# Kernel tuning notes

Measured on AMD Instinct MI355X. Metric: run time of the kernel, lower is better.

Reference implementation:

```python
import jax, jax.numpy as jnp
import numpy as np

B, N, D, H = 4, 2048, 768, 12
DK = D // H  # 64

def setup_inputs() -> dict:
    key = jax.random.key(0)
    ks = jax.random.split(key, 7)
    f = lambda k, shape: jax.random.normal(k, shape, dtype=jnp.float32)
    return {
        "Q": f(ks[0], (B, N, D)),
        "K": f(ks[1], (B, N, D)),
        "V": f(ks[2], (B, N, D)),
        "w_q": f(ks[3], (D, D)) * 0.02,
        "w_k": f(ks[4], (D, D)) * 0.02,
        "w_v": f(ks[5], (D, D)) * 0.02,
        "w_o": f(ks[6], (D, D)) * 0.02,
    }

def reference(Q, K, V, w_q, w_k, w_v, w_o):
    # Linear with bias=False: y = x @ W.T, W is [out, in]
    def proj(x, w):
        # [B, N, D] -> [B, H, N, DK]
        y = jnp.einsum('bnd,ed->bne', x, w)
        return y.reshape(B, N, H, DK).transpose(0, 2, 1, 3)
    q = proj(Q, w_q)
    k = proj(K, w_k)
    v = proj(V, w_v)
    scale = 1.0 / jnp.sqrt(jnp.float32(DK))
    scores = jnp.einsum('bhqd,bhkd->bhqk', q, k) * scale  # [B,H,N,N]
    weights = jax.nn.softmax(scores, axis=-1)
    out = jnp.einsum('bhqk,bhkd->bhqd', weights, v)  # [B,H,N,DK]
    out = out.transpose(0, 2, 1, 3).reshape(B, N, D)
    return jnp.einsum('bnd,ed->bne', out, w_o)
```

## Files before the change

kernel.cpp:

```cpp
#include <hip/hip_runtime.h>

typedef unsigned short ushortT;
typedef __attribute__((ext_vector_type(8))) short bf16x8;
typedef __attribute__((ext_vector_type(4))) float f32x4;
typedef __attribute__((ext_vector_type(16))) float f32x16;
typedef __attribute__((ext_vector_type(2))) int i32x2;

#define QSCALE 0.18033688011112042f

__device__ __forceinline__ unsigned short f2bf(float f) {
  unsigned int u = __float_as_uint(f);
  u += 0x7FFFu + ((u >> 16) & 1u);
  return (unsigned short)(u >> 16);
}
__device__ __forceinline__ unsigned short f2bf_fast(float f) {
  unsigned int u = __float_as_uint(f) + 0x8000u;
  return (unsigned short)(u >> 16);
}

__device__ __forceinline__ void gl16(const void* g, void* l) {
  __builtin_amdgcn_global_load_lds(
      (const __attribute__((address_space(1))) void*)g,
      (__attribute__((address_space(3))) void*)l, 16, 0, 0);
}

__device__ __forceinline__ unsigned cvtpk(float lo, float hi) {
  unsigned r;
  asm("v_cvt_pk_bf16_f32 %0, %1, %2" : "=v"(r) : "v"(lo), "v"(hi));
  return r;
}

__global__ __launch_bounds__(256) void cvt_w(
    const float* __restrict__ w0, const float* __restrict__ w1,
    const float* __restrict__ w2, const float* __restrict__ w3,
    ushortT* bw0, ushortT* bw1, ushortT* bw2, ushortT* bw3) {
  int t = blockIdx.y;
  const float* src; ushortT* dst;
  switch (t) {
    case 0: src = w0; dst = bw0; break;
    case 1: src = w1; dst = bw1; break;
    case 2: src = w2; dst = bw2; break;
    default: src = w3; dst = bw3; break;
  }
  int i = (blockIdx.x * 256 + threadIdx.x) * 4;
  float4 f = *(const float4*)(src + i);
  ushort4 o = make_ushort4(f2bf(f.x), f2bf(f.y), f2bf(f.z), f2bf(f.w));
  *(ushort4*)(dst + i) = o;
}

__global__ __launch_bounds__(256) void gemm_qkv(
    const float* __restrict__ fxq, const float* __restrict__ fxk,
    const float* __restrict__ fxv,
    const ushortT* __restrict__ bwq, const ushortT* __restrict__ bwk,
    const ushortT* __restrict__ bwv,
    ushortT* qp, ushortT* kp, ushortT* vtp) {
  constexpr int K = 768;
  __shared__ __attribute__((aligned(16))) ushortT As[128 * 32];
  __shared__ __attribute__((aligned(16))) ushortT Bs[128 * 32];
  const int tid = threadIdx.x;
  const int w = tid >> 6, l = tid & 63;
  const int z = blockIdx.z;
  const int d = blockIdx.x;
  const int bx = (d & 7) * 48 + (d >> 3);
  const float*   Fx = (z == 0) ? fxq : (z == 1 ? fxk : fxv);
  const ushortT* Wb = (z == 0) ? bwq : (z == 1 ? bwk : bwv);
  int m0, n0;
  if (z < 2) { m0 = (bx / 6) * 128; n0 = (bx % 6) * 128; }
  else       { m0 = (bx % 6) * 128; n0 = (bx / 6) * 128; }
  const float*   Fb = Fx + (size_t)(z < 2 ? m0 : n0) * K;
  const ushortT* Gb = Wb + (size_t)(z < 2 ? n0 : m0) * K;
  ushortT* Fl = (z < 2) ? As : Bs;
  ushortT* Gl = (z < 2) ? Bs : As;

  f32x4 acc[4][4] = {};
  const int wr = w >> 1, wc = w & 1;
  const int lg = l >> 4, li = l & 15;
  const int srow = tid >> 2, scol = (tid & 3) * 8;

  for (int k0 = 0; k0 < K; k0 += 32) {
    const float* p0 = Fb + (size_t)srow * K + k0 + scol;
    const float* p1 = Fb + (size_t)(64 + srow) * K + k0 + scol;
    float4 a0 = *(const float4*)p0;
    float4 a1 = *(const float4*)(p0 + 4);
    float4 b0 = *(const float4*)p1;
    float4 b1 = *(const float4*)(p1 + 4);
    gl16(Gb + (size_t)srow * K + (k0 + scol),        (char*)Gl + w * 1024);
    gl16(Gb + (size_t)(64 + srow) * K + (k0 + scol), (char*)Gl + 4096 + w * 1024);
    union { unsigned u[4]; bf16x8 v; } pa, pb;
    pa.u[0] = cvtpk(a0.x, a0.y); pa.u[1] = cvtpk(a0.z, a0.w);
    pa.u[2] = cvtpk(a1.x, a1.y); pa.u[3] = cvtpk(a1.z, a1.w);
    pb.u[0] = cvtpk(b0.x, b0.y); pb.u[1] = cvtpk(b0.z, b0.w);
    pb.u[2] = cvtpk(b1.x, b1.y); pb.u[3] = cvtpk(b1.z, b1.w);
    *(bf16x8*)&Fl[srow * 32 + scol]        = pa.v;
    *(bf16x8*)&Fl[(64 + srow) * 32 + scol] = pb.v;
    __syncthreads();
    bf16x8 af[4], bfr[4];
#pragma unroll
    for (int mi = 0; mi < 4; ++mi)
      af[mi] = *(const bf16x8*)&As[(wr * 64 + mi * 16 + li) * 32 + lg * 8];
#pragma unroll
    for (int ni = 0; ni < 4; ++ni)
      bfr[ni] = *(const bf16x8*)&Bs[(wc * 64 + ni * 16 + li) * 32 + lg * 8];
#pragma unroll
    for (int mi = 0; mi < 4; ++mi)
#pragma unroll
      for (int ni = 0; ni < 4; ++ni)
        acc[mi][ni] = __builtin_amdgcn_mfma_f32_16x16x32_bf16(af[mi], bfr[ni], acc[mi][ni], 0, 0, 0);
    __syncthreads();
  }

  const float sc = (z == 0) ? QSCALE : 1.0f;
  ushortT* dst0 = (z == 0) ? qp : kp;
#pragma unroll
  for (int mi = 0; mi < 4; ++mi) {
#pragma unroll
    for (int ni = 0; ni < 4; ++ni) {
#pragma unroll
      for (int r = 0; r < 4; ++r) {
        int m = m0 + wr * 64 + mi * 16 + lg * 4 + r;
        int n = n0 + wc * 64 + ni * 16 + li;
        float val = acc[mi][ni][r];
        if (z < 2) {
          int b = m >> 11, nn = m & 2047, hh = n >> 6, dk = n & 63;
          dst0[(((size_t)(b * 12 + hh)) * 2048 + nn) * 64 + dk] = f2bf_fast(val * sc);
        } else {
          vtp[(size_t)m * 8192 + n] = f2bf_fast(val);
        }
      }
    }
  }
}

__global__ __launch_bounds__(256) void gemm_out(
    const ushortT* __restrict__ A0, const ushortT* __restrict__ B0, float* O0) {
  constexpr int K = 768;
  __shared__ __attribute__((aligned(16))) ushortT As[128 * 32];
  __shared__ __attribute__((aligned(16))) ushortT Bs[128 * 32];
  const int tid = threadIdx.x;
  const int w = tid >> 6, l = tid & 63;
  const int d = blockIdx.x;
  const int flat = (d & 7) * 48 + (d >> 3);
  const int m0 = (flat / 6) * 128, n0 = (flat % 6) * 128;
  const ushortT* Ab = A0 + (size_t)m0 * K;
  const ushortT* Bb = B0 + (size_t)n0 * K;

  f32x4 acc[4][4] = {};
  const int wr = w >> 1, wc = w & 1;
  const int lg = l >> 4, li = l & 15;
  const int srow = tid >> 2, scol = (tid & 3) * 8;

  for (int k0 = 0; k0 < K; k0 += 32) {
    gl16(Ab + (size_t)srow * K + (k0 + scol),        &As[w * 512]);
    gl16(Ab + (size_t)(64 + srow) * K + (k0 + scol), &As[2048 + w * 512]);
    gl16(Bb + (size_t)srow * K + (k0 + scol),        &Bs[w * 512]);
    gl16(Bb + (size_t)(64 + srow) * K + (k0 + scol), &Bs[2048 + w * 512]);
    __syncthreads();
    bf16x8 af[4], bfr[4];
#pragma unroll
    for (int mi = 0; mi < 4; ++mi)
      af[mi] = *(const bf16x8*)&As[(wr * 64 + mi * 16 + li) * 32 + lg * 8];
#pragma unroll
    for (int ni = 0; ni < 4; ++ni)
      bfr[ni] = *(const bf16x8*)&Bs[(wc * 64 + ni * 16 + li) * 32 + lg * 8];
#pragma unroll
    for (int mi = 0; mi < 4; ++mi)
#pragma unroll
      for (int ni = 0; ni < 4; ++ni)
        acc[mi][ni] = __builtin_amdgcn_mfma_f32_16x16x32_bf16(af[mi], bfr[ni], acc[mi][ni], 0, 0, 0);
    __syncthreads();
  }

#pragma unroll
  for (int mi = 0; mi < 4; ++mi)
#pragma unroll
    for (int ni = 0; ni < 4; ++ni)
#pragma unroll
      for (int r = 0; r < 4; ++r) {
        int m = m0 + wr * 64 + mi * 16 + lg * 4 + r;
        int n = n0 + wc * 64 + ni * 16 + li;
        O0[(size_t)m * 768 + n] = acc[mi][ni][r];
      }
}

__global__ __launch_bounds__(256, 3) void attn(
    const ushortT* __restrict__ qp, const ushortT* __restrict__ kp,
    const ushortT* __restrict__ vtp, ushortT* __restrict__ ao) {
  __shared__ __attribute__((aligned(16))) ushortT Ks[128 * 64];
  __shared__ __attribute__((aligned(16))) ushortT Vs[2 * 64 * 64];
  __shared__ __attribute__((aligned(16))) ushortT Ot[4][32 * 72];
  const int tid = threadIdx.x;
  const int w = tid >> 6, l = tid & 63;
  const int lq = l & 31, h = l >> 5;

  const int flat = blockIdx.y * 16 + blockIdx.x;
  const int head = (flat & 7) * 6 + (flat >> 7);
  const int qt = (flat >> 3) & 15;
  const int bb = head / 12, hh = head % 12;
  const size_t hb = (size_t)head * 2048 * 64;
  const int q0 = qt * 128 + w * 32;

  const ushortT* kbase = kp + hb;
  const ushortT* vbase = vtp + (size_t)(hh * 64) * 8192 + (size_t)bb * 2048;

  const int srow8 = l >> 3;
  const int scol = ((l & 7) ^ srow8) << 3;

#define STAGE(kt)                                                              \
  {                                                                            \
    _Pragma("unroll") for (int j = 0; j < 4; ++j) {                            \
      int rk = (w << 5) + (j << 3) + srow8;                                    \
      gl16(kbase + (size_t)((kt) * 128 + rk) * 64 + scol,                      \
           (char*)Ks + ((w << 5) + (j << 3)) * 128);                           \
      int rv = ((w & 1) << 5) + (j << 3) + srow8;                              \
      gl16(vbase + (size_t)rv * 8192 + (kt) * 128 + (w >> 1) * 64 + scol,      \
           (char*)Vs + (w >> 1) * 8192 + (((w & 1) << 5) + (j << 3)) * 128);   \
    }                                                                          \
  }

  bf16x8 bq[4];
#pragma unroll
  for (int c = 0; c < 4; ++c)
    bq[c] = *(const bf16x8*)&qp[hb + (size_t)(q0 + lq) * 64 + c * 16 + h * 8];

  bf16x8 ones;
#pragma unroll
  for (int e = 0; e < 8; ++e) ones[e] = (short)0x3F80;

  f32x16 oa0 = {}, oa1 = {};
  f32x16 asum = {};
  const int lq7 = lq & 7;

  for (int kt = 0; kt < 16; ++kt) {
    STAGE(kt);
    __syncthreads();

#pragma unroll
    for (int khalf = 0; khalf < 2; ++khalf) {
      const char* kbuf = (const char*)Ks + khalf * 8192;
      const char* vbuf = (const char*)Vs + khalf * 8192;

      f32x16 s0 = {}, s1 = {};
      __builtin_amdgcn_s_setprio(1);
#pragma unroll
      for (int c = 0; c < 4; ++c) {
        bf16x8 a0 = *(const bf16x8*)(kbuf + lq * 128 + (((2 * c + h) ^ lq7) << 4));
        s0 = __builtin_amdgcn_mfma_f32_32x32x16_bf16(a0, bq[c], s0, 0, 0, 0);
      }
#pragma unroll
      for (int c = 0; c < 4; ++c) {
        bf16x8 a1 = *(const bf16x8*)(kbuf + (32 + lq) * 128 + (((2 * c + h) ^ lq7) << 4));
        s1 = __builtin_amdgcn_mfma_f32_32x32x16_bf16(a1, bq[c], s1, 0, 0, 0);
      }
      __builtin_amdgcn_s_setprio(0);

#pragma unroll
      for (int r = 0; r < 16; ++r) s0[r] = exp2f(s0[r]);
#pragma unroll
      for (int r = 0; r < 16; ++r) s1[r] = exp2f(s1[r]);

      unsigned c8[16];
#pragma unroll
      for (int n = 0; n < 8; ++n) c8[n]     = cvtpk(s0[2 * n], s0[2 * n + 1]);
#pragma unroll
      for (int n = 0; n < 8; ++n) c8[8 + n] = cvtpk(s1[2 * n], s1[2 * n + 1]);

      __builtin_amdgcn_s_setprio(1);
#pragma unroll
      for (int kcg = 0; kcg < 4; ++kcg) {
        const unsigned* cc = &c8[(kcg >> 1) * 8 + (kcg & 1) * 4];
        i32x2 rA = __builtin_amdgcn_permlane32_swap((int)cc[0], (int)cc[2], false, false);
        i32x2 rB = __builtin_amdgcn_permlane32_swap((int)cc[1], (int)cc[3], false, false);
        union { int u4[4]; bf16x8 v8; } pb;
        pb.u4[0] = rA[0]; pb.u4[1] = rB[0]; pb.u4[2] = rA[1]; pb.u4[3] = rB[1];
        bf16x8 av0 = *(const bf16x8*)(vbuf + lq * 128 + (((2 * kcg + h) ^ lq7) << 4));
        bf16x8 av1 = *(const bf16x8*)(vbuf + (32 + lq) * 128 + (((2 * kcg + h) ^ lq7) << 4));
        oa0 = __builtin_amdgcn_mfma_f32_32x32x16_bf16(av0, pb.v8, oa0, 0, 0, 0);
        oa1 = __builtin_amdgcn_mfma_f32_32x32x16_bf16(av1, pb.v8, oa1, 0, 0, 0);
        asum = __builtin_amdgcn_mfma_f32_32x32x16_bf16(ones, pb.v8, asum, 0, 0, 0);
      }
      __builtin_amdgcn_s_setprio(0);
    }

    __syncthreads();
  }
#undef STAGE

  ushortT* ot = Ot[w];
  float inv = 1.f / asum[0];
#pragma unroll
  for (int r4 = 0; r4 < 4; ++r4) {
    int d2 = 8 * r4 + 4 * h;
    uint2 p0, p1;
    p0.x = cvtpk(oa0[4 * r4 + 0] * inv, oa0[4 * r4 + 1] * inv);
    p0.y = cvtpk(oa0[4 * r4 + 2] * inv, oa0[4 * r4 + 3] * inv);
    p1.x = cvtpk(oa1[4 * r4 + 0] * inv, oa1[4 * r4 + 1] * inv);
    p1.y = cvtpk(oa1[4 * r4 + 2] * inv, oa1[4 * r4 + 3] * inv);
    *(uint2*)&ot[lq * 72 + d2]      = p0;
    *(uint2*)&ot[lq * 72 + 32 + d2] = p1;
  }
  asm volatile("s_waitcnt lgkmcnt(0)" ::: "memory");
  __builtin_amdgcn_sched_barrier(0);
  const int tq = l >> 1, dh = (l & 1) * 32;
  const size_t orow = ((size_t)(bb * 2048 + q0 + tq)) * 768 + hh * 64 + dh;
#pragma unroll
  for (int c = 0; c < 4; ++c) {
    bf16x8 x = *(const bf16x8*)&ot[tq * 72 + dh + c * 8];
    *(bf16x8*)&ao[orow + c * 8] = x;
  }
}

extern "C" void kernel_launch(void* const* d_in, const int* in_sizes, int n_in,
                              void* d_out, int out_size, void* d_ws, size_t ws_size,
                              hipStream_t stream) {
  const float* Q  = (const float*)d_in[0];
  const float* K_ = (const float*)d_in[1];
  const float* V  = (const float*)d_in[2];
  const float* wq = (const float*)d_in[3];
  const float* wk = (const float*)d_in[4];
  const float* wv = (const float*)d_in[5];
  const float* wo = (const float*)d_in[6];

  ushortT* bwq = (ushortT*)d_ws;
  ushortT* bwk = bwq + (size_t)768 * 768;
  ushortT* bwv = bwk + (size_t)768 * 768;
  ushortT* bwo = bwv + (size_t)768 * 768;
  ushortT* qp  = bwo + (size_t)768 * 768;
  ushortT* kp  = qp  + (size_t)8192 * 768;
  ushortT* vtp = kp  + (size_t)8192 * 768;
  ushortT* aob = vtp + (size_t)8192 * 768;

  cvt_w<<<dim3(576, 4), 256, 0, stream>>>(wq, wk, wv, wo, bwq, bwk, bwv, bwo);

  gemm_qkv<<<dim3(384, 1, 3), 256, 0, stream>>>(Q, K_, V, bwq, bwk, bwv,
                                                qp, kp, vtp);

  attn<<<dim3(16, 48), 256, 0, stream>>>(qp, kp, vtp, aob);

  gemm_out<<<384, 256, 0, stream>>>(aob, bwo, (float*)d_out);
}
```

Measured before the change: 163.1 us.

## Double-buffer 64-key K/V tiles in attention and write output directly

The attention loop moves from one 128-key single-buffered K/V tile with two barriers per iteration to two 64-key buffers, so the global-to-LDS copy of the next tile runs while the current tile is computed. The epilogue drops the LDS transpose staging buffer and stores 8-byte packed bf16 pieces straight to global memory. LDS use stays the same with the Ot buffer removed, and occupancy is unchanged. The risks are uncoalesced 8-byte output stores and twice as many loop iterations and barriers. The prefetch is also issued with no explicit vmcnt wait before the next tile is read, so correctness relies on the barrier's implicit waits.

Result: slower. 167.5 us (+2.7%).

```diff
diff --git a/kernel.cpp b/kernel.cpp
--- a/kernel.cpp
+++ b/kernel.cpp
@@ -185,9 +185,8 @@
 __global__ __launch_bounds__(256, 3) void attn(
     const ushortT* __restrict__ qp, const ushortT* __restrict__ kp,
     const ushortT* __restrict__ vtp, ushortT* __restrict__ ao) {
-  __shared__ __attribute__((aligned(16))) ushortT Ks[128 * 64];
-  __shared__ __attribute__((aligned(16))) ushortT Vs[2 * 64 * 64];
-  __shared__ __attribute__((aligned(16))) ushortT Ot[4][32 * 72];
+  __shared__ __attribute__((aligned(16))) ushortT Ks[2][64 * 64];
+  __shared__ __attribute__((aligned(16))) ushortT Vs[2][64 * 64];
   const int tid = threadIdx.x;
   const int w = tid >> 6, l = tid & 63;
   const int lq = l & 31, h = l >> 5;
@@ -205,15 +204,14 @@
   const int srow8 = l >> 3;
   const int scol = ((l & 7) ^ srow8) << 3;
 
-#define STAGE(kt)                                                              \
+#define STAGE(buf, kt)                                                         \
   {                                                                            \
-    _Pragma("unroll") for (int j = 0; j < 4; ++j) {                            \
-      int rk = (w << 5) + (j << 3) + srow8;                                    \
-      gl16(kbase + (size_t)((kt) * 128 + rk) * 64 + scol,                      \
-           (char*)Ks + ((w << 5) + (j << 3)) * 128);                           \
-      int rv = ((w & 1) << 5) + (j << 3) + srow8;                              \
-      gl16(vbase + (size_t)rv * 8192 + (kt) * 128 + (w >> 1) * 64 + scol,      \
-           (char*)Vs + (w >> 1) * 8192 + (((w & 1) << 5) + (j << 3)) * 128);   \
+    _Pragma("unroll") for (int j = 0; j < 2; ++j) {                            \
+      int r = (w << 4) + (j << 3) + srow8;                                     \
+      gl16(kbase + (size_t)((kt) * 64 + r) * 64 + scol,                        \
+           (char*)Ks[buf] + ((w << 4) + (j << 3)) * 128);                      \
+      gl16(vbase + (size_t)r * 8192 + (kt) * 64 + scol,                        \
+           (char*)Vs[buf] + ((w << 4) + (j << 3)) * 128);                      \
     }                                                                          \
   }
 
@@ -230,82 +228,73 @@
   f32x16 asum = {};
   const int lq7 = lq & 7;
 
-  for (int kt = 0; kt < 16; ++kt) {
-    STAGE(kt);
-    __syncthreads();
-
-#pragma unroll
-    for (int khalf = 0; khalf < 2; ++khalf) {
-      const char* kbuf = (const char*)Ks + khalf * 8192;
-      const char* vbuf = (const char*)Vs + khalf * 8192;
-
-      f32x16 s0 = {}, s1 = {};
-      __builtin_amdgcn_s_setprio(1);
-#pragma unroll
-      for (int c = 0; c < 4; ++c) {
-        bf16x8 a0 = *(const bf16x8*)(kbuf + lq * 128 + (((2 * c + h) ^ lq7) << 4));
-        s0 = __builtin_amdgcn_mfma_f32_32x32x16_bf16(a0, bq[c], s0, 0, 0, 0);
-      }
-#pragma unroll
-      for (int c = 0; c < 4; ++c) {
-        bf16x8 a1 = *(const bf16x8*)(kbuf + (32 + lq) * 128 + (((2 * c + h) ^ lq7) << 4));
-        s1 = __builtin_amdgcn_mfma_f32_32x32x16_bf16(a1, bq[c], s1, 0, 0, 0);
-      }
-      __builtin_amdgcn_s_setprio(0);
-
-#pragma unroll
-      for (int r = 0; r < 16; ++r) s0[r] = exp2f(s0[r]);
-#pragma unroll
-      for (int r = 0; r < 16; ++r) s1[r] = exp2f(s1[r]);
-
-      unsigned c8[16];
-#pragma unroll
-      for (int n = 0; n < 8; ++n) c8[n]     = cvtpk(s0[2 * n], s0[2 * n + 1]);
-#pragma unroll
-      for (int n = 0; n < 8; ++n) c8[8 + n] = cvtpk(s1[2 * n], s1[2 * n + 1]);
-
-      __builtin_amdgcn_s_setprio(1);
-#pragma unroll
-      for (int kcg = 0; kcg < 4; ++kcg) {
-        const unsigned* cc = &c8[(kcg >> 1) * 8 + (kcg & 1) * 4];
-        i32x2 rA = __builtin_amdgcn_permlane32_swap((int)cc[0], (int)cc[2], false, false);
-        i32x2 rB = __builtin_amdgcn_permlane32_swap((int)cc[1], (int)cc[3], false, false);
-        union { int u4[4]; bf16x8 v8; } pb;
-        pb.u4[0] = rA[0]; pb.u4[1] = rB[0]; pb.u4[2] = rA[1]; pb.u4[3] = rB[1];
-        bf16x8 av0 = *(const bf16x8*)(vbuf + lq * 128 + (((2 * kcg + h) ^ lq7) << 4));
-        bf16x8 av1 = *(const bf16x8*)(vbuf + (32 + lq) * 128 + (((2 * kcg + h) ^ lq7) << 4));
-        oa0 = __builtin_amdgcn_mfma_f32_32x32x16_bf16(av0, pb.v8, oa0, 0, 0, 0);
-        oa1 = __builtin_amdgcn_mfma_f32_32x32x16_bf16(av1, pb.v8, oa1, 0, 0, 0);
-        asum = __builtin_amdgcn_mfma_f32_32x32x16_bf16(ones, pb.v8, asum, 0, 0, 0);
-      }
-      __builtin_amdgcn_s_setprio(0);
+  STAGE(0, 0);
+  __syncthreads();
+
+  int cur = 0;
+  for (int kt = 0; kt < 32; ++kt) {
+    if (kt + 1 < 32) STAGE(cur ^ 1, kt + 1);
+
+    const char* kbuf = (const char*)Ks[cur];
+    const char* vbuf = (const char*)Vs[cur];
+
+    f32x16 s0 = {}, s1 = {};
+    __builtin_amdgcn_s_setprio(1);
+#pragma unroll
+    for (int c = 0; c < 4; ++c) {
+      bf16x8 a0 = *(const bf16x8*)(kbuf + lq * 128 + (((2 * c + h) ^ lq7) << 4));
+      s0 = __builtin_amdgcn_mfma_f32_32x32x16_bf16(a0, bq[c], s0, 0, 0, 0);
     }
-
-    __syncthreads();
+#pragma unroll
+    for (int c = 0; c < 4; ++c) {
+      bf16x8 a1 = *(const bf16x8*)(kbuf + (32 + lq) * 128 + (((2 * c + h) ^ lq7) << 4));
+      s1 = __builtin_amdgcn_mfma_f32_32x32x16_bf16(a1, bq[c], s1, 0, 0, 0);
+    }
+    __builtin_amdgcn_s_setprio(0);
+
+#pragma unroll
+    for (int r = 0; r < 16; ++r) s0[r] = exp2f(s0[r]);
+#pragma unroll
+    for (int r = 0; r < 16; ++r) s1[r] = exp2f(s1[r]);
+
+    unsigned c8[16];
+#pragma unroll
+    for (int n = 0; n < 8; ++n) c8[n]     = cvtpk(s0[2 * n], s0[2 * n + 1]);
+#pragma unroll
+    for (int n = 0; n < 8; ++n) c8[8 + n] = cvtpk(s1[2 * n], s1[2 * n + 1]);
+
+    __builtin_amdgcn_s_setprio(1);
+#pragma unroll
+    for (int kcg = 0; kcg < 4; ++kcg) {
+      const unsigned* cc = &c8[(kcg >> 1) * 8 + (kcg & 1) * 4];
+      i32x2 rA = __builtin_amdgcn_permlane32_swap((int)cc[0], (int)cc[2], false, false);
+      i32x2 rB = __builtin_amdgcn_permlane32_swap((int)cc[1], (int)cc[3], false, false);
+      union { int u4[4]; bf16x8 v8; } pb;
+      pb.u4[0] = rA[0]; pb.u4[1] = rB[0]; pb.u4[2] = rA[1]; pb.u4[3] = rB[1];
+      bf16x8 av0 = *(const bf16x8*)(vbuf + lq * 128 + (((2 * kcg + h) ^ lq7) << 4));
+      bf16x8 av1 = *(const bf16x8*)(vbuf + (32 + lq) * 128 + (((2 * kcg + h) ^ lq7) << 4));
+      oa0 = __builtin_amdgcn_mfma_f32_32x32x16_bf16(av0, pb.v8, oa0, 0, 0, 0);
+      oa1 = __builtin_amdgcn_mfma_f32_32x32x16_bf16(av1, pb.v8, oa1, 0, 0, 0);
+      asum = __builtin_amdgcn_mfma_f32_32x32x16_bf16(ones, pb.v8, asum, 0, 0, 0);
+    }
+    __builtin_amdgcn_s_setprio(0);
+
+    __syncthreads();
+    cur ^= 1;
   }
 #undef STAGE
 
-  ushortT* ot = Ot[w];
   float inv = 1.f / asum[0];
+  const size_t orow = ((size_t)(bb * 2048 + q0 + lq)) * 768 + hh * 64 + 4 * h;
 #pragma unroll
   for (int r4 = 0; r4 < 4; ++r4) {
-    int d2 = 8 * r4 + 4 * h;
     uint2 p0, p1;
     p0.x = cvtpk(oa0[4 * r4 + 0] * inv, oa0[4 * r4 + 1] * inv);
     p0.y = cvtpk(oa0[4 * r4 + 2] * inv, oa0[4 * r4 + 3] * inv);
     p1.x = cvtpk(oa1[4 * r4 + 0] * inv, oa1[4 * r4 + 1] * inv);
     p1.y = cvtpk(oa1[4 * r4 + 2] * inv, oa1[4 * r4 + 3] * inv);
-    *(uint2*)&ot[lq * 72 + d2]      = p0;
-    *(uint2*)&ot[lq * 72 + 32 + d2] = p1;
-  }
-  asm volatile("s_waitcnt lgkmcnt(0)" ::: "memory");
-  __builtin_amdgcn_sched_barrier(0);
-  const int tq = l >> 1, dh = (l & 1) * 32;
-  const size_t orow = ((size_t)(bb * 2048 + q0 + tq)) * 768 + hh * 64 + dh;
-#pragma unroll
-  for (int c = 0; c < 4; ++c) {
-    bf16x8 x = *(const bf16x8*)&ot[tq * 72 + dh + c * 8];
-    *(bf16x8*)&ao[orow + c * 8] = x;
+    *(uint2*)&ao[orow + 8 * r4]      = p0;
+    *(uint2*)&ao[orow + 32 + 8 * r4] = p1;
   }
 }
 
```
